# Kernel optimization log

Measured on AMD Instinct MI355X. Metric: run time of the kernel, lower is better.

Reference implementation:

```python
import jax, jax.numpy as jnp
import numpy as np

# Problem sizes
N, D, B = 4096, 2048, 64  # nodes, feature dim, sequential samples
# LARFDSSOM hyperparameters (from __init__ defaults)
A_T = 0.3          # activation threshold
DSBETA = 1e-4      # moving-average rate
E_B = 0.5          # winner learning rate
E_N = 0.01 * E_B   # neighbor learning rate (e_n is multiplied by e_b in __init__)
EPS_DS = 0.01      # relevance smoothing


def setup_inputs() -> dict:
    key = jax.random.key(0)
    k0, k1, k2, k3, k4 = jax.random.split(key, 5)
    return {
        "x": jax.random.uniform(k0, (B, D), jnp.float32),
        "weights": jax.random.uniform(k1, (N, D), jnp.float32),
        "moving_avg": jax.random.uniform(k2, (N, D), jnp.float32),
        "relevances": jax.random.uniform(k3, (N, D), jnp.float32),
        "wins": jnp.zeros((N,), jnp.float32),
        "neighbors": jax.random.randint(k4, (N, N), 0, 2) > 0,
    }


def _som_steps(x, weights, moving_avg, relevances, wins, neighbors):
    """Sequential LARFDSSOM update_map over B samples (codebook at max size,
    so the add_node branch is structurally impossible and the per-sample step
    is either 'update winner + neighbors' or a no-op)."""
    node_ids = jnp.arange(weights.shape[0])

    def step(state, w):
        W, M, R, wn = state
        diff = w[None, :] - W                          # [N, D]
        # weighted_distance + activation
        dists = jnp.sum(R * diff * diff, axis=1)       # [N]
        rel_sum = jnp.sum(R, axis=1)                   # [N]
        act = rel_sum / (rel_sum + dists + 1e-7)
        winner = jnp.argmax(act)
        do_upd = act[winner] >= A_T                    # else no-op (codebook full)
        is_winner = node_ids == winner
        is_nb = neighbors[winner] & (~is_winner)
        # per-node learning rate: e_b for winner, e_n for neighbors, 0 otherwise
        lr = jnp.where(is_winner, E_B, jnp.where(is_nb, E_N, 0.0))[:, None]  # [N, 1]
        # update_node (vectorized over all nodes, masked below)
        dist_abs = jnp.abs(diff)
        M_new = lr * DSBETA * dist_abs + (1.0 - lr * DSBETA) * M
        mx = jnp.max(M_new, axis=1, keepdims=True)
        mn = jnp.min(M_new, axis=1, keepdims=True)
        av = jnp.mean(M_new, axis=1, keepdims=True)
        denom = EPS_DS * (mx - mn)
        # denom == 0 -> original produces NaN then sets relevance to 1.0
        arg = jnp.clip((M_new - av) / jnp.where(denom == 0.0, 1.0, denom), -80.0, 80.0)
        R_new = jnp.where(denom == 0.0, 1.0, 1.0 / (1.0 + jnp.exp(arg)))
        W_new = W + lr * diff
        m = (do_upd & (lr[:, 0] > 0.0))[:, None]       # rows actually touched
        W = jnp.where(m, W_new, W)
        M = jnp.where(m, M_new, M)
        R = jnp.where(m, R_new, R)
        wn = wn + jnp.where(is_winner & do_upd, 1.0, 0.0)
        return (W, M, R, wn), None

    (W, M, R, wn), _ = jax.lax.scan(step, (weights, moving_avg, relevances, wins), x)
    return W


def reference(x, weights, moving_avg, relevances, wins, neighbors):
    return _som_steps(x, weights, moving_avg, relevances, wins, neighbors)
```

## Files before the change

### kernel.cpp

```cpp
#include <hip/hip_runtime.h>
#include <hip/hip_cooperative_groups.h>
#include <cstddef>

namespace cg = cooperative_groups;

#define NN 4096
#define DD 2048
#define BB 64
#define RPB 8
#define GRID_BLKS (NN / RPB)

constexpr float kAT     = 0.3f;
constexpr float kDSBETA = 1e-4f;
constexpr float kEB     = 0.5f;
constexpr float kEN     = 0.005f;
constexpr float kEPS    = 0.01f;

__device__ __forceinline__ float wave_sum_f(float v) {
#pragma unroll
    for (int o = 32; o; o >>= 1) v += __shfl_xor(v, o, 64);
    return v;
}
__device__ __forceinline__ double wave_sum_d(double v) {
#pragma unroll
    for (int o = 32; o; o >>= 1) v += __shfl_xor(v, o, 64);
    return v;
}
__device__ __forceinline__ float wave_max_f(float v) {
#pragma unroll
    for (int o = 32; o; o >>= 1) v = fmaxf(v, __shfl_xor(v, o, 64));
    return v;
}
__device__ __forceinline__ float wave_min_f(float v) {
#pragma unroll
    for (int o = 32; o; o >>= 1) v = fminf(v, __shfl_xor(v, o, 64));
    return v;
}
__device__ __forceinline__ unsigned long long wave_max_u64(unsigned long long v) {
#pragma unroll
    for (int o = 32; o; o >>= 1) {
        const unsigned long long u = __shfl_xor(v, o, 64);
        v = (u > v) ? u : v;
    }
    return v;
}

__global__ void detect_nb(const unsigned char* __restrict__ nb, unsigned* __restrict__ flag) {
    unsigned v = 0;
    const int i0 = threadIdx.x * 256;
    for (int i = 0; i < 256; i++) {
        const int idx = i0 + i;
        if ((idx & 3) != 0) v |= nb[idx];
    }
    if (v != 0) atomicOr(flag, 1u);
}

__global__ __launch_bounds__(256, 2) void som_all(
    const float* __restrict__ x,
    const float* __restrict__ W0,
    const float* __restrict__ M0,
    const float* __restrict__ R0,
    const unsigned char* __restrict__ nbb,
    const unsigned* __restrict__ flag,
    float* __restrict__ Wout,
    unsigned long long* __restrict__ part)
{
    cg::grid_group grid = cg::this_grid();
    const int tid  = threadIdx.x;
    const int wid  = tid >> 6;
    const int lane = tid & 63;
    const int n0   = (int)blockIdx.x * RPB;
    const int col  = tid * 8;

    __shared__ double sdd[2][RPB][4];
    __shared__ float  sf[3][4];
    __shared__ unsigned long long skk[RPB];

    const bool nb_byte = (*flag != 0);
    const int* nbi = (const int*)nbb;

    float w[RPB][8], r[RPB][8], m[RPB][8], xcur[8];

#pragma unroll
    for (int row = 0; row < RPB; ++row) {
        const size_t base = (size_t)(n0 + row) * DD + col;
        *(float4*)(&w[row][0]) = *(const float4*)(W0 + base);
        *(float4*)(&w[row][4]) = *(const float4*)(W0 + base + 4);
        *(float4*)(&r[row][0]) = *(const float4*)(R0 + base);
        *(float4*)(&r[row][4]) = *(const float4*)(R0 + base + 4);
        *(float4*)(&m[row][0]) = *(const float4*)(M0 + base);
        *(float4*)(&m[row][4]) = *(const float4*)(M0 + base + 4);
    }
    *(float4*)(xcur)     = *(const float4*)(x + col);
    *(float4*)(xcur + 4) = *(const float4*)(x + col + 4);

    auto act_phase = [&](int slot) {
#pragma unroll
        for (int row = 0; row < RPB; ++row) {
            double pd = 0.0, ps = 0.0;
#pragma unroll
            for (int j = 0; j < 8; ++j) {
                const double d  = (double)xcur[j] - (double)w[row][j];
                const double rj = (double)r[row][j];
                pd += rj * d * d;
                ps += rj;
            }
            pd = wave_sum_d(pd); ps = wave_sum_d(ps);
            if (lane == 0) { sdd[0][row][wid] = pd; sdd[1][row][wid] = ps; }
        }
        __syncthreads();
        if (tid < RPB) {
            const int row = tid;
            const double td = sdd[0][row][0] + sdd[0][row][1] + sdd[0][row][2] + sdd[0][row][3];
            const double tr = sdd[1][row][0] + sdd[1][row][1] + sdd[1][row][2] + sdd[1][row][3];
            const double act = tr / (tr + td + 1e-7);
            const unsigned long long ab = (unsigned long long)__double_as_longlong(act);
            skk[row] = (ab & ~0xFFFULL) | (unsigned long long)(4095 - (n0 + row));
        }
        __syncthreads();
        if (tid == 0) {
            unsigned long long k = skk[0];
#pragma unroll
            for (int i = 1; i < RPB; ++i) k = (skk[i] > k) ? skk[i] : k;
            atomicMax(&part[(size_t)slot * 64 * 8 + (size_t)(blockIdx.x & 63) * 8], k);
        }
    };

    act_phase(0);

    for (int t = 0; t < BB; ++t) {
        grid.sync();

        unsigned long long k = __hip_atomic_load(
            &part[(size_t)t * 64 * 8 + (size_t)lane * 8],
            __ATOMIC_RELAXED, __HIP_MEMORY_SCOPE_AGENT);
        k = wave_max_u64(k);
        const double act_w = __longlong_as_double((long long)(k & ~0xFFFULL));
        const int winner   = 4095 - (int)(k & 0xFFFULL);

        if (act_w >= (double)kAT) {
#pragma unroll
            for (int row = 0; row < RPB; ++row) {
                const int n = n0 + row;
                float lr = 0.0f;
                if (n == winner) {
                    lr = kEB;
                } else {
                    const size_t off = (size_t)winner * NN + n;
                    const bool isnb = nb_byte ? (nbb[off] != 0) : (nbi[off] != 0);
                    if (isnb) lr = kEN;
                }
                if (lr != 0.0f) {
                    const float c1 = lr * kDSBETA;
                    const float c2 = 1.0f - c1;
                    float psum = 0.0f, pmx = -INFINITY, pmn = INFINITY;
#pragma unroll
                    for (int j = 0; j < 8; ++j) {
                        const float d  = xcur[j] - w[row][j];
                        const float mv = c1 * fabsf(d) + c2 * m[row][j];
                        w[row][j] += lr * d;
                        m[row][j] = mv;
                        psum += mv;
                        pmx = fmaxf(pmx, mv);
                        pmn = fminf(pmn, mv);
                    }
                    psum = wave_sum_f(psum); pmx = wave_max_f(pmx); pmn = wave_min_f(pmn);
                    if (lane == 0) { sf[0][wid] = psum; sf[1][wid] = pmx; sf[2][wid] = pmn; }
                    __syncthreads();
                    const float ts  = sf[0][0] + sf[0][1] + sf[0][2] + sf[0][3];
                    const float tmx = fmaxf(fmaxf(sf[1][0], sf[1][1]), fmaxf(sf[1][2], sf[1][3]));
                    const float tmn = fminf(fminf(sf[2][0], sf[2][1]), fminf(sf[2][2], sf[2][3]));
                    __syncthreads();
                    const float av    = ts * (1.0f / (float)DD);
                    const float denom = kEPS * (tmx - tmn);
                    if (denom == 0.0f) {
#pragma unroll
                        for (int j = 0; j < 8; ++j) r[row][j] = 1.0f;
                    } else {
#pragma unroll
                        for (int j = 0; j < 8; ++j) {
                            float a = (m[row][j] - av) / denom;
                            a = fminf(fmaxf(a, -80.0f), 80.0f);
                            r[row][j] = 1.0f / (1.0f + expf(a));
                        }
                    }
                }
            }
        }

        if (t < BB - 1) {
            const size_t xb = (size_t)(t + 1) * DD + col;
            *(float4*)(xcur)     = *(const float4*)(x + xb);
            *(float4*)(xcur + 4) = *(const float4*)(x + xb + 4);
            act_phase(t + 1);
        }
    }

#pragma unroll
    for (int row = 0; row < RPB; ++row) {
        const size_t base = (size_t)(n0 + row) * DD + col;
        *(float4*)(Wout + base)     = *(float4*)(&w[row][0]);
        *(float4*)(Wout + base + 4) = *(float4*)(&w[row][4]);
    }
}

__global__ __launch_bounds__(256) void som_step(
    const float* __restrict__ x_upd, const float* __restrict__ x_act,
    float* __restrict__ W, float* __restrict__ M, float* __restrict__ R,
    const void* __restrict__ nb, const unsigned* __restrict__ flag,
    const unsigned long long* __restrict__ part_upd,
    unsigned long long* __restrict__ part_act)
{
    const int n   = blockIdx.x;
    const int tid = threadIdx.x;
    __shared__ float  sred[3][4];
    __shared__ double sredd[2][4];

    float lr = 0.0f;
    if (part_upd != nullptr) {
        unsigned long long k = part_upd[(size_t)(tid & 63) * 8];
        k = wave_max_u64(k);
        const double act_w = __longlong_as_double((long long)(k & ~0xFFFULL));
        const int winner   = 4095 - (int)(k & 0xFFFULL);
        if (act_w >= (double)kAT) {
            if (n == winner) lr = kEB;
            else {
                const size_t off = (size_t)winner * NN + n;
                const bool isnb = (*flag != 0)
                    ? (((const unsigned char*)nb)[off] != 0)
                    : (((const int*)nb)[off] != 0);
                if (isnb) lr = kEN;
            }
        }
    }
    const bool next = (x_act != nullptr);
    if (lr == 0.0f && !next) return;

    const size_t rowoff = (size_t)n * DD + (size_t)tid * 8;
    const size_t xoff   = (size_t)tid * 8;
    float w[8], r[8];
    *(float4*)(w)     = *(const float4*)(W + rowoff);
    *(float4*)(w + 4) = *(const float4*)(W + rowoff + 4);

    if (lr != 0.0f) {
        float m[8], xu[8], mnew[8];
        *(float4*)(m)      = *(const float4*)(M + rowoff);
        *(float4*)(m + 4)  = *(const float4*)(M + rowoff + 4);
        *(float4*)(xu)     = *(const float4*)(x_upd + xoff);
        *(float4*)(xu + 4) = *(const float4*)(x_upd + xoff + 4);
        const float c1 = lr * kDSBETA, c2 = 1.0f - c1;
        float psum = 0.0f, pmx = -INFINITY, pmn = INFINITY;
#pragma unroll
        for (int j = 0; j < 8; j++) {
            const float d = xu[j] - w[j];
            w[j] += lr * d;
            const float mv = c1 * fabsf(d) + c2 * m[j];
            mnew[j] = mv; psum += mv;
            pmx = fmaxf(pmx, mv); pmn = fminf(pmn, mv);
        }
        psum = wave_sum_f(psum); pmx = wave_max_f(pmx); pmn = wave_min_f(pmn);
        const int wid = tid >> 6, lane = tid & 63;
        if (lane == 0) { sred[0][wid] = psum; sred[1][wid] = pmx; sred[2][wid] = pmn; }
        __syncthreads();
        const float ts  = sred[0][0] + sred[0][1] + sred[0][2] + sred[0][3];
        const float tmx = fmaxf(fmaxf(sred[1][0], sred[1][1]), fmaxf(sred[1][2], sred[1][3]));
        const float tmn = fminf(fminf(sred[2][0], sred[2][1]), fminf(sred[2][2], sred[2][3]));
        __syncthreads();
        const float av = ts * (1.0f / (float)DD);
        const float denom = kEPS * (tmx - tmn);
        if (denom == 0.0f) {
#pragma unroll
            for (int j = 0; j < 8; j++) r[j] = 1.0f;
        } else {
#pragma unroll
            for (int j = 0; j < 8; j++) {
                float a = (mnew[j] - av) / denom;
                a = fminf(fmaxf(a, -80.0f), 80.0f);
                r[j] = 1.0f / (1.0f + expf(a));
            }
        }
        *(float4*)(W + rowoff)     = *(float4*)(w);
        *(float4*)(W + rowoff + 4) = *(float4*)(w + 4);
        *(float4*)(M + rowoff)     = *(float4*)(mnew);
        *(float4*)(M + rowoff + 4) = *(float4*)(mnew + 4);
        *(float4*)(R + rowoff)     = *(float4*)(r);
        *(float4*)(R + rowoff + 4) = *(float4*)(r + 4);
    } else {
        *(float4*)(r)     = *(const float4*)(R + rowoff);
        *(float4*)(r + 4) = *(const float4*)(R + rowoff + 4);
    }

    if (next) {
        float xn[8];
        *(float4*)(xn)     = *(const float4*)(x_act + xoff);
        *(float4*)(xn + 4) = *(const float4*)(x_act + xoff + 4);
        double pd = 0.0, ps = 0.0;
#pragma unroll
        for (int j = 0; j < 8; j++) {
            const double d  = (double)xn[j] - (double)w[j];
            const double rj = (double)r[j];
            pd += rj * d * d; ps += rj;
        }
        pd = wave_sum_d(pd); ps = wave_sum_d(ps);
        const int wid = tid >> 6, lane = tid & 63;
        if (lane == 0) { sredd[0][wid] = pd; sredd[1][wid] = ps; }
        __syncthreads();
        if (tid == 0) {
            const double td = sredd[0][0] + sredd[0][1] + sredd[0][2] + sredd[0][3];
            const double tr = sredd[1][0] + sredd[1][1] + sredd[1][2] + sredd[1][3];
            const double act = tr / (tr + td + 1e-7);
            const unsigned long long ab = (unsigned long long)__double_as_longlong(act);
            const unsigned long long kk = (ab & ~0xFFFULL) | (unsigned long long)(4095 - n);
            atomicMax(&part_act[(size_t)(n & 63) * 8], kk);
        }
    }
}

extern "C" void kernel_launch(void* const* d_in, const int* in_sizes, int n_in,
                              void* d_out, int out_size, void* d_ws, size_t ws_size,
                              hipStream_t stream) {
    const float*         x   = (const float*)d_in[0];
    const float*         W0  = (const float*)d_in[1];
    float*               M   = (float*)d_in[2];
    float*               R   = (float*)d_in[3];
    const unsigned char* nbb = (const unsigned char*)d_in[5];
    float*               W   = (float*)d_out;

    unsigned long long* part = (unsigned long long*)d_ws;
    const size_t part_bytes  = (size_t)66 * 64 * 8 * sizeof(unsigned long long);
    unsigned*           flagp = (unsigned*)((char*)d_ws + part_bytes);

    hipMemsetAsync(d_ws, 0, part_bytes + 64, stream);
    detect_nb<<<1, 256, 0, stream>>>(nbb, flagp);

    int occ = 0;
    hipError_t qerr = hipOccupancyMaxActiveBlocksPerMultiprocessor(
        &occ, (const void*)som_all, 256, 0);
    bool coop_ok = (qerr == hipSuccess && occ >= 2);

    if (coop_ok) {
        const float* xp = x; const float* w0p = W0; const float* m0p = (const float*)M;
        const float* r0p = (const float*)R; const unsigned char* nbp = nbb;
        const unsigned* fp = flagp; float* wp = W; unsigned long long* pp = part;
        void* args[] = { &xp, &w0p, &m0p, &r0p, &nbp, &fp, &wp, &pp };
        hipError_t lerr = hipLaunchCooperativeKernel((const void*)som_all,
                                                     dim3(GRID_BLKS), dim3(256),
                                                     args, 0, stream);
        if (lerr == hipSuccess) return;
    }

    hipMemcpyAsync(W, W0, sizeof(float) * (size_t)NN * DD, hipMemcpyDeviceToDevice, stream);
    som_step<<<NN, 256, 0, stream>>>(nullptr, x, W, M, R, nbb, flagp, nullptr, part);
    for (int t = 0; t < BB; t++) {
        const float* xu = x + (size_t)t * DD;
        const float* xa = (t < BB - 1) ? (x + (size_t)(t + 1) * DD) : nullptr;
        const unsigned long long* pu = part + (size_t)t * 64 * 8;
        unsigned long long*       pa = (t < BB - 1) ? (part + (size_t)(t + 1) * 64 * 8) : nullptr;
        som_step<<<NN, 256, 0, stream>>>(xu, xa, W, M, R, nbb, flagp, pu, pa);
    }
}
```

Measured before the change: 1.662 ms.

## Replace cooperative grid.sync with per-step atomic counter barrier in persistent kernel

Drops the cooperative-groups grid barrier and launches the persistent kernel normally. Each block bumps one of eight padded per-step counters with release semantics, and one wave per block spins with acquire loads and s_sleep until all blocks have arrived, then reads the winner key. This targets the cost of 64 full grid.sync calls by having each block wait only on the counters for its own step. Without a cooperative launch, all 512 blocks are no longer guaranteed to be co-resident, so the kernel relies on the occupancy check, and the spin loop gives up after a fixed iteration cap.

```diff
diff --git a/kernel.cpp b/kernel.cpp
--- a/kernel.cpp
+++ b/kernel.cpp
@@ -1,14 +1,11 @@
 #include <hip/hip_runtime.h>
-#include <hip/hip_cooperative_groups.h>
 #include <cstddef>
-
-namespace cg = cooperative_groups;
 
 #define NN 4096
 #define DD 2048
 #define BB 64
 #define RPB 8
-#define GRID_BLKS (NN / RPB)
+#define NBLK (NN / RPB)
 
 constexpr float kAT     = 0.3f;
 constexpr float kDSBETA = 1e-4f;
@@ -55,7 +52,7 @@
     if (v != 0) atomicOr(flag, 1u);
 }
 
-__global__ __launch_bounds__(256, 2) void som_all(
+__global__ __launch_bounds__(256, 2) void som_persist(
     const float* __restrict__ x,
     const float* __restrict__ W0,
     const float* __restrict__ M0,
@@ -63,9 +60,9 @@
     const unsigned char* __restrict__ nbb,
     const unsigned* __restrict__ flag,
     float* __restrict__ Wout,
-    unsigned long long* __restrict__ part)
+    unsigned long long* __restrict__ part,
+    unsigned* __restrict__ cnt)
 {
-    cg::grid_group grid = cg::this_grid();
     const int tid  = threadIdx.x;
     const int wid  = tid >> 6;
     const int lane = tid & 63;
@@ -75,6 +72,7 @@
     __shared__ double sdd[2][RPB][4];
     __shared__ float  sf[3][4];
     __shared__ unsigned long long skk[RPB];
+    __shared__ unsigned long long sKey;
 
     const bool nb_byte = (*flag != 0);
     const int* nbi = (const int*)nbb;
@@ -122,19 +120,40 @@
             unsigned long long k = skk[0];
 #pragma unroll
             for (int i = 1; i < RPB; ++i) k = (skk[i] > k) ? skk[i] : k;
-            atomicMax(&part[(size_t)slot * 64 * 8 + (size_t)(blockIdx.x & 63) * 8], k);
-        }
+            atomicMax(&part[((size_t)slot * 64 + (blockIdx.x & 63)) * 8], k);
+            __hip_atomic_fetch_add(&cnt[((size_t)slot * 8 + (blockIdx.x & 7)) * 16], 1u,
+                                   __ATOMIC_RELEASE, __HIP_MEMORY_SCOPE_AGENT);
+        }
+        __syncthreads();
     };
 
     act_phase(0);
 
     for (int t = 0; t < BB; ++t) {
-        grid.sync();
-
-        unsigned long long k = __hip_atomic_load(
-            &part[(size_t)t * 64 * 8 + (size_t)lane * 8],
-            __ATOMIC_RELAXED, __HIP_MEMORY_SCOPE_AGENT);
-        k = wave_max_u64(k);
+        if (wid == 0) {
+            int it = 0;
+            while (true) {
+                unsigned c = 0;
+                if (lane < 8)
+                    c = __hip_atomic_load(&cnt[((size_t)t * 8 + lane) * 16],
+                                          __ATOMIC_ACQUIRE, __HIP_MEMORY_SCOPE_AGENT);
+                c += __shfl_xor(c, 1, 64);
+                c += __shfl_xor(c, 2, 64);
+                c += __shfl_xor(c, 4, 64);
+                c = __shfl(c, 0, 64);
+                if (c >= (unsigned)NBLK) break;
+                if (++it > 2000000) break;
+                __builtin_amdgcn_s_sleep(2);
+            }
+            unsigned long long k = __hip_atomic_load(
+                &part[((size_t)t * 64 + lane) * 8],
+                __ATOMIC_RELAXED, __HIP_MEMORY_SCOPE_AGENT);
+            k = wave_max_u64(k);
+            if (lane == 0) sKey = k;
+        }
+        __syncthreads();
+        const unsigned long long k = sKey;
+        __syncthreads();
         const double act_w = __longlong_as_double((long long)(k & ~0xFFFULL));
         const int winner   = 4095 - (int)(k & 0xFFFULL);
 
@@ -328,25 +347,19 @@
 
     unsigned long long* part = (unsigned long long*)d_ws;
     const size_t part_bytes  = (size_t)66 * 64 * 8 * sizeof(unsigned long long);
-    unsigned*           flagp = (unsigned*)((char*)d_ws + part_bytes);
-
-    hipMemsetAsync(d_ws, 0, part_bytes + 64, stream);
+    unsigned* cnt   = (unsigned*)((char*)d_ws + part_bytes);
+    const size_t cnt_bytes = (size_t)BB * 8 * 16 * sizeof(unsigned);
+    unsigned* flagp = (unsigned*)((char*)d_ws + part_bytes + cnt_bytes);
+
+    hipMemsetAsync(d_ws, 0, part_bytes + cnt_bytes + 64, stream);
     detect_nb<<<1, 256, 0, stream>>>(nbb, flagp);
 
     int occ = 0;
     hipError_t qerr = hipOccupancyMaxActiveBlocksPerMultiprocessor(
-        &occ, (const void*)som_all, 256, 0);
-    bool coop_ok = (qerr == hipSuccess && occ >= 2);
-
-    if (coop_ok) {
-        const float* xp = x; const float* w0p = W0; const float* m0p = (const float*)M;
-        const float* r0p = (const float*)R; const unsigned char* nbp = nbb;
-        const unsigned* fp = flagp; float* wp = W; unsigned long long* pp = part;
-        void* args[] = { &xp, &w0p, &m0p, &r0p, &nbp, &fp, &wp, &pp };
-        hipError_t lerr = hipLaunchCooperativeKernel((const void*)som_all,
-                                                     dim3(GRID_BLKS), dim3(256),
-                                                     args, 0, stream);
-        if (lerr == hipSuccess) return;
+        &occ, (const void*)som_persist, 256, 0);
+    if (qerr == hipSuccess && occ >= 2) {
+        som_persist<<<NBLK, 256, 0, stream>>>(x, W0, M, R, nbb, flagp, W, part, cnt);
+        return;
     }
 
     hipMemcpyAsync(W, W0, sizeof(float) * (size_t)NN * DD, hipMemcpyDeviceToDevice, stream);
```

New measurement: 1.660 ms. About the same (-0.1%).
